# Kernel optimization log

Hardware: AMD Instinct MI355X
Metric: run time of the kernel (lower is better)

The kernel has to match this reference:

```python
import jax, jax.numpy as jnp
import numpy as np

MAX_USERS = 100000
T = 2            # edge_type_count
D = 100          # edge_dim
B = 512
IN_DIM = 200
OUT_DIM = 200
PARTS = [[3, 15], [3, 15, 105, 945]]   # per-schema neighbor partition sizes
RAND_PARTS = [3, 15]
TOTAL_P = sum(PARTS[0]) + sum(PARTS[1])


def _layernorm(x, g, b, eps=1e-6):
    mu = x.mean(axis=-1, keepdims=True)
    var = ((x - mu) ** 2).mean(axis=-1, keepdims=True)
    return (x - mu) / jnp.sqrt(var + eps) * g + b


def _mha(x, Wq, Wk, Wv, Wf, g, b):
    # single-head attention over the second-to-last axis (n_head=1, d_k=d_v=D).
    # NOTE: original only layer-norms q (k, v use the raw input); residual add at end.
    residual = x
    q = _layernorm(x, g, b) @ Wq
    k = x @ Wk
    v = x @ Wv
    attn = jax.nn.softmax(jnp.einsum('...qd,...kd->...qk', q / jnp.sqrt(D), k), axis=-1)
    out = jnp.einsum('...qk,...kd->...qd', attn, v) @ Wf
    return out + residual, attn


def _mean_agg(Ws, Wn, self_x, neigh_x):
    # GraphSAGE-style mean aggregator: relu(concat(self @ Ws, mean(neigh) @ Wn)).
    # neigh_x has shape [N*r, D]; reshape to [N, r, D] and mean over the fanout r.
    n, d = self_x.shape
    neigh_mean = neigh_x.reshape(n, -1, d).mean(axis=1)
    return jax.nn.relu(jnp.concatenate([self_x @ Ws, neigh_mean @ Wn], axis=-1))


def _schema_view(idx, parts, Wself, Wneigh, type_embed, nodeids, neigh_s):
    # neigh_s: [B, T, sum(parts)] node ids for meta-path idx. Returns [B, T, D].
    # Faithful to type_embed[neigh][:, :, :, :, idx, :][:, t, :, t, :] but gathers
    # only the needed (type t, schema idx) slice instead of the huge dense tensor.
    chunks = jnp.split(neigh_s, np.cumsum(parts)[:-1].tolist(), axis=2)
    specs = []
    for t in range(T):
        feats = [type_embed[nodeids, t, idx]]                    # [B, D]
        for c in chunks:
            feats.append(type_embed[c[:, t, :], t, idx].reshape(-1, D))
        for l in range(len(parts)):
            feats = [_mean_agg(Wself[l], Wneigh[l], feats[k], feats[k + 1])
                     for k in range(len(feats) - 1)]
        specs.append(feats[0])
    return jnp.stack(specs, axis=1)


def setup_inputs() -> dict:
    ks = jax.random.split(jax.random.key(0), 32)
    unif = lambda i, s: jax.random.uniform(ks[i], s, dtype=jnp.float32, minval=-1.0, maxval=1.0)
    nrm = lambda i, s, sc=0.1: jax.random.normal(ks[i], s, dtype=jnp.float32) * sc
    inp = {}
    inp['nodeids'] = jax.random.randint(ks[0], (B,), 0, MAX_USERS)
    inp['edgetype'] = jnp.stack([jnp.arange(B), jax.random.randint(ks[1], (B,), 0, T)])
    inp['neighbors'] = jax.random.randint(ks[2], (B, T, TOTAL_P), 0, MAX_USERS)
    inp['random_neighbors'] = jax.random.randint(ks[3], (B, sum(RAND_PARTS)), 0, MAX_USERS)
    inp['base_embed'] = unif(4, (MAX_USERS, IN_DIM))
    inp['type_embed'] = unif(5, (MAX_USERS, T, len(PARTS), D))
    inp['rw_embed'] = unif(6, (MAX_USERS, D))
    inp['reflect'] = nrm(7, (T, D, OUT_DIM), 1.0 / float(np.sqrt(IN_DIM)))
    inp['agg0_self'] = nrm(8, (2, D, D // 2)); inp['agg0_neigh'] = nrm(9, (2, D, D // 2))
    inp['agg1_self'] = nrm(10, (4, D, D // 2)); inp['agg1_neigh'] = nrm(11, (4, D, D // 2))
    inp['rand_self'] = nrm(12, (2, D, D // 2)); inp['rand_neigh'] = nrm(13, (2, D, D // 2))
    inp['vWq'] = nrm(14, (D, D)); inp['vWk'] = nrm(15, (D, D)); inp['vWv'] = nrm(16, (D, D)); inp['vWf'] = nrm(17, (D, D))
    inp['vg'] = jnp.ones((D,), jnp.float32); inp['vb'] = jnp.zeros((D,), jnp.float32)
    inp['mWq'] = nrm(18, (D, D)); inp['mWk'] = nrm(19, (D, D)); inp['mWv'] = nrm(20, (D, D)); inp['mWf'] = nrm(21, (D, D))
    inp['mg'] = jnp.ones((D,), jnp.float32); inp['mb'] = jnp.zeros((D,), jnp.float32)
    return inp


def reference(nodeids, edgetype, neighbors, random_neighbors, base_embed, type_embed,
              rw_embed, reflect, agg0_self, agg0_neigh, agg1_self, agg1_neigh,
              rand_self, rand_neigh, vWq, vWk, vWv, vWf, vg, vb,
              mWq, mWk, mWv, mWf, mg, mb):
    # per-metapath views [B, T, D]
    spec0 = _schema_view(0, PARTS[0], agg0_self, agg0_neigh, type_embed, nodeids,
                         neighbors[:, :, :sum(PARTS[0])])
    spec1 = _schema_view(1, PARTS[1], agg1_self, agg1_neigh, type_embed, nodeids,
                         neighbors[:, :, sum(PARTS[0]):])
    # random-walk view [B, D]
    feats = [rw_embed[nodeids]]
    for c in jnp.split(random_neighbors, np.cumsum(RAND_PARTS)[:-1].tolist(), axis=1):
        feats.append(rw_embed[c].reshape(-1, D))
    for l in range(len(RAND_PARTS)):
        feats = [_mean_agg(rand_self[l], rand_neigh[l], feats[k], feats[k + 1])
                 for k in range(len(feats) - 1)]
    rview = feats[0]
    mv = jnp.stack([spec0, spec1], axis=1)                                   # [B, 2, T, D]
    mv = jnp.concatenate([mv, jnp.broadcast_to(rview[:, None, None, :], (B, 1, T, D))], axis=1)  # [B, 3, T, D]
    mv, _ = _mha(mv, vWq, vWk, vWv, vWf, vg, vb)                             # view attn over type axis T
    mt, _ = _mha(jnp.swapaxes(mv, 1, 2), mWq, mWk, mWv, mWf, mg, mb)         # meta attn over view axis
    pooled = jnp.swapaxes(mt, 1, 2).mean(axis=1)                             # [B, T, D]
    sel = pooled[edgetype[0], edgetype[1]]                                   # [B, D]
    out = jnp.einsum('bd,bdo->bo', sel, reflect[edgetype[1]])                # [B, OUT_DIM]
    res = base_embed[nodeids] + out
    return res / jnp.maximum(jnp.linalg.norm(res, axis=1, keepdims=True), 1e-12)
```

## Files before the change

### kernel.cpp

```cpp
#include <hip/hip_runtime.h>
#include <math.h>


#define NBATCH 512
#define TOTALP 1086
#define RPB 32
#define XSTR 204

struct Seg {
  const float* emb;
  const float* selfp;
  const float* neighp;
  const int*   ids_s;
  const int*   ids_n;
  const float* Ws;
  const float* Wn;
  float*       outp;
  int ss, so;
  int ns, no;
  int estride;
  int ostride;
  int c;
  int r;
  int blk_begin;
};

struct KArgs { Seg seg[14]; int n; };

__global__ __launch_bounds__(256, 5) void agg_kernel(KArgs P) {
  __shared__ float xsh[RPB * XSTR];
  __shared__ int   ids_s_sh[RPB];
  __shared__ int   ids_n_sh[RPB * 9];

  const int blk = blockIdx.x, tid = threadIdx.x;
  int si = 0;
  for (int i = 1; i < P.n; ++i)
    if (blk >= P.seg[i].blk_begin) si = i;
  const Seg sg = P.seg[si];
  const int j0 = (blk - sg.blk_begin) * RPB;
  const int c = sg.c, r = sg.r;

  if (sg.emb) {
    if (tid < RPB) {
      int j = j0 + tid, b = j / c, pos = j - b * c;
      ids_s_sh[tid] = sg.ids_s[(long)b * sg.ss + sg.so + pos];
    }
    for (int u = tid; u < RPB * r; u += 256) {
      int row = u / r, q = u - row * r;
      int j = j0 + row, b = j / c, pos = j - b * c;
      ids_n_sh[u] = sg.ids_n[(long)b * sg.ns + sg.no + pos * r + q];
    }
  }
  __syncthreads();

  const float rinv = 1.f / (float)r;
  for (int u = tid; u < RPB * 25; u += 256) {
    int row = u / 25, q4 = (u - row * 25) * 4;
    float sx, sy, sz, sw, mx = 0.f, my = 0.f, mz = 0.f, mw = 0.f;
    if (sg.emb) {
      const float4 s4 = *(const float4*)(sg.emb + (long)ids_s_sh[row] * sg.estride + q4);
      sx = s4.x; sy = s4.y; sz = s4.z; sw = s4.w;
      for (int rr = 0; rr < r; ++rr) {
        const float4 t = *(const float4*)(sg.emb + (long)ids_n_sh[row * r + rr] * sg.estride + q4);
        mx += t.x; my += t.y; mz += t.z; mw += t.w;
      }
    } else {
      long j = j0 + row;
      const float4 s4 = *(const float4*)(sg.selfp + j * 100 + q4);
      sx = s4.x; sy = s4.y; sz = s4.z; sw = s4.w;
      for (int rr = 0; rr < r; ++rr) {
        const float4 t = *(const float4*)(sg.neighp + (j * r + rr) * 100 + q4);
        mx += t.x; my += t.y; mz += t.z; mw += t.w;
      }
    }
    float4 sv; sv.x = sx; sv.y = sy; sv.z = sz; sv.w = sw;
    float4 mv; mv.x = mx * rinv; mv.y = my * rinv; mv.z = mz * rinv; mv.w = mw * rinv;
    *(float4*)&xsh[row * XSTR + q4]       = sv;
    *(float4*)&xsh[row * XSTR + 100 + q4] = mv;
  }
  __syncthreads();

  if (tid < 224) {
    const int rg = tid / 28, cq = tid - rg * 28;
    const int cl = (cq < 14) ? cq : cq - 14;
    const float* Wg = (cq < 14) ? sg.Ws : sg.Wn;
    const int c0 = (cl < 13) ? 4 * cl : 0;
    const int c1 = (cl < 12) ? c0 + 2 : c0;
    const int xoff = (cq < 14) ? 0 : 100;
    float acc[4][4];
#pragma unroll
    for (int i = 0; i < 4; ++i) { acc[i][0] = acc[i][1] = acc[i][2] = acc[i][3] = 0.f; }
    const float* xb = &xsh[(rg * 4) * XSTR + xoff];
#pragma unroll 4
    for (int e = 0; e < 100; ++e) {
      const float2 w0 = *(const float2*)&Wg[e * 50 + c0];
      const float2 w1 = *(const float2*)&Wg[e * 50 + c1];
#pragma unroll
      for (int i = 0; i < 4; ++i) {
        const float a = xb[i * XSTR + e];
        acc[i][0] = fmaf(a, w0.x, acc[i][0]);
        acc[i][1] = fmaf(a, w0.y, acc[i][1]);
        acc[i][2] = fmaf(a, w1.x, acc[i][2]);
        acc[i][3] = fmaf(a, w1.y, acc[i][3]);
      }
    }
    if (cl < 13) {
      const int cbase = (cq < 14 ? 0 : 50) + 4 * cl;
      for (int i = 0; i < 4; ++i) {
        const long j = j0 + rg * 4 + i;
        float* op = sg.outp + j * (long)sg.ostride + cbase;
        if (cl < 12) {
          float4 o;
          o.x = fmaxf(acc[i][0], 0.f); o.y = fmaxf(acc[i][1], 0.f);
          o.z = fmaxf(acc[i][2], 0.f); o.w = fmaxf(acc[i][3], 0.f);
          *(float4*)op = o;
        } else {
          op[0] = fmaxf(acc[i][0], 0.f);
          op[1] = fmaxf(acc[i][1], 0.f);
        }
      }
    }
  }
}

__device__ __forceinline__ void attn_step(
    float* xs, int base, int rs, int n,
    const float* Wq, const float* Wk, const float* Wv, const float* Wf,
    const float* g, const float* bb,
    float* ln, float* qq, float* kk, float* vv, float* ot,
    float* sc, float* musd, float* wsh, int tid)
{
  if (tid < n) {
    float mu = 0.f;
    for (int d = 0; d < 100; ++d) mu += xs[base + tid * rs + d];
    mu *= 0.01f;
    float var = 0.f;
    for (int d = 0; d < 100; ++d) {
      float t = xs[base + tid * rs + d] - mu; var = fmaf(t, t, var);
    }
    var *= 0.01f;
    musd[tid * 2]     = mu;
    musd[tid * 2 + 1] = rsqrtf(var + 1e-6f);
  }
  __syncthreads();
  for (int o = tid; o < n * 100; o += 128) {
    int i = o / 100, d = o - i * 100;
    ln[o] = (xs[base + i * rs + d] - musd[i * 2]) * musd[i * 2 + 1] * g[d] + bb[d];
  }
  __syncthreads();

  const bool act = tid < n * 25;
  const int  i   = tid / 25;
  const int  d4  = 4 * (tid - i * 25);
  float aq[4] = {0,0,0,0}, ak[4] = {0,0,0,0}, av[4] = {0,0,0,0};
  for (int ch = 0; ch < 2; ++ch) {
    for (int u = tid; u < 1250; u += 128) {
      int el = u / 25, dd = 4 * (u - el * 25);
      *(float4*)&wsh[el * 300 + dd]       = *(const float4*)&Wq[(ch * 50 + el) * 100 + dd];
      *(float4*)&wsh[el * 300 + 100 + dd] = *(const float4*)&Wk[(ch * 50 + el) * 100 + dd];
      *(float4*)&wsh[el * 300 + 200 + dd] = *(const float4*)&Wv[(ch * 50 + el) * 100 + dd];
    }
    __syncthreads();
    if (act) {
      for (int el = 0; el < 50; ++el) {
        const float lnv = ln[i * 100 + ch * 50 + el];
        const float xv  = xs[base + i * rs + ch * 50 + el];
        const float4 wq = *(const float4*)&wsh[el * 300 + d4];
        const float4 wk = *(const float4*)&wsh[el * 300 + 100 + d4];
        const float4 wv = *(const float4*)&wsh[el * 300 + 200 + d4];
        aq[0] = fmaf(lnv, wq.x, aq[0]); aq[1] = fmaf(lnv, wq.y, aq[1]);
        aq[2] = fmaf(lnv, wq.z, aq[2]); aq[3] = fmaf(lnv, wq.w, aq[3]);
        ak[0] = fmaf(xv,  wk.x, ak[0]); ak[1] = fmaf(xv,  wk.y, ak[1]);
        ak[2] = fmaf(xv,  wk.z, ak[2]); ak[3] = fmaf(xv,  wk.w, ak[3]);
        av[0] = fmaf(xv,  wv.x, av[0]); av[1] = fmaf(xv,  wv.y, av[1]);
        av[2] = fmaf(xv,  wv.z, av[2]); av[3] = fmaf(xv,  wv.w, av[3]);
      }
    }
    __syncthreads();
  }
  if (act) {
#pragma unroll
    for (int jj = 0; jj < 4; ++jj) {
      qq[i * 100 + d4 + jj] = aq[jj];
      kk[i * 100 + d4 + jj] = ak[jj];
      vv[i * 100 + d4 + jj] = av[jj];
    }
  }
  __syncthreads();

  if (tid < n * n) {
    int qi = tid / n, u = tid - qi * n;
    float s = 0.f;
    for (int d = 0; d < 100; ++d) s = fmaf(qq[qi * 100 + d], kk[u * 100 + d], s);
    sc[tid] = s * 0.1f;
  }
  __syncthreads();
  if (tid < n) {
    float mx = sc[tid * n];
    for (int u = 1; u < n; ++u) mx = fmaxf(mx, sc[tid * n + u]);
    float sm = 0.f;
    for (int u = 0; u < n; ++u) {
      float e = expf(sc[tid * n + u] - mx); sc[tid * n + u] = e; sm += e;
    }
    float inv = 1.f / sm;
    for (int u = 0; u < n; ++u) sc[tid * n + u] *= inv;
  }
  __syncthreads();
  for (int o = tid; o < n * 100; o += 128) {
    int ii = o / 100, d = o - ii * 100;
    float a = 0.f;
    for (int u = 0; u < n; ++u) a = fmaf(sc[ii * n + u], vv[u * 100 + d], a);
    ot[o] = a;
  }
  __syncthreads();

  float af[4] = {0,0,0,0};
  for (int ch = 0; ch < 2; ++ch) {
    for (int u = tid; u < 1250; u += 128) {
      int el = u / 25, dd = 4 * (u - el * 25);
      *(float4*)&wsh[el * 100 + dd] = *(const float4*)&Wf[(ch * 50 + el) * 100 + dd];
    }
    __syncthreads();
    if (act) {
      for (int el = 0; el < 50; ++el) {
        const float ov = ot[i * 100 + ch * 50 + el];
        const float4 wf = *(const float4*)&wsh[el * 100 + d4];
        af[0] = fmaf(ov, wf.x, af[0]); af[1] = fmaf(ov, wf.y, af[1]);
        af[2] = fmaf(ov, wf.z, af[2]); af[3] = fmaf(ov, wf.w, af[3]);
      }
    }
    __syncthreads();
  }
  if (act) {
#pragma unroll
    for (int jj = 0; jj < 4; ++jj)
      xs[base + i * rs + d4 + jj] += af[jj];
  }
  __syncthreads();
}

__global__ __launch_bounds__(128) void attn_final_kernel(
    const float* __restrict__ spec, const float* __restrict__ rview,
    const int* __restrict__ nodeids, const int* __restrict__ edgetype,
    const float* __restrict__ base_embed, const float* __restrict__ reflect,
    const float* vWq, const float* vWk, const float* vWv, const float* vWf,
    const float* vg, const float* vb,
    const float* mWq, const float* mWk, const float* mWv, const float* mWf,
    const float* mg, const float* mb,
    float* __restrict__ out)
{
  __shared__ float xs[600], ln[300], qq[300], kk[300], vv[300], ot[300];
  __shared__ float sc[9], musd[6], r200[200], pooled[200], nrmv[1];
  __shared__ float wsh[15000];
  const int b = blockIdx.x, tid = threadIdx.x;

  for (int o = tid; o < 600; o += 128) {
    int v = o / 200, rem = o - v * 200;
    xs[o] = (v < 2) ? spec[(long)b * 400 + o] : rview[(long)b * 100 + (rem % 100)];
  }
  __syncthreads();

  for (int v = 0; v < 3; ++v)
    attn_step(xs, v * 200, 100, 2, vWq, vWk, vWv, vWf, vg, vb,
              ln, qq, kk, vv, ot, sc, musd, wsh, tid);
  for (int t = 0; t < 2; ++t)
    attn_step(xs, t * 100, 200, 3, mWq, mWk, mWv, mWf, mg, mb,
              ln, qq, kk, vv, ot, sc, musd, wsh, tid);

  for (int o = tid; o < 200; o += 128)
    pooled[o] = (xs[o] + xs[200 + o] + xs[400 + o]) * (1.f / 3.f);
  __syncthreads();

  const int  et  = edgetype[NBATCH + b];
  const long nid = nodeids[b];

  float ar[4] = {0,0,0,0};
  if (tid < 50) {
    const float4 be = *(const float4*)&base_embed[nid * 200 + 4 * tid];
    ar[0] = be.x; ar[1] = be.y; ar[2] = be.z; ar[3] = be.w;
  }
  for (int ch = 0; ch < 2; ++ch) {
    for (int u = tid; u < 2500; u += 128) {
      int dl = u / 50, oo = 4 * (u - dl * 50);
      *(float4*)&wsh[dl * 200 + oo] =
          *(const float4*)&reflect[((long)et * 100 + ch * 50 + dl) * 200 + oo];
    }
    __syncthreads();
    if (tid < 50) {
      for (int dl = 0; dl < 50; ++dl) {
        const float pv = pooled[et * 100 + ch * 50 + dl];
        const float4 rv = *(const float4*)&wsh[dl * 200 + 4 * tid];
        ar[0] = fmaf(pv, rv.x, ar[0]); ar[1] = fmaf(pv, rv.y, ar[1]);
        ar[2] = fmaf(pv, rv.z, ar[2]); ar[3] = fmaf(pv, rv.w, ar[3]);
      }
    }
    __syncthreads();
  }
  if (tid < 50) {
    r200[4 * tid]     = ar[0]; r200[4 * tid + 1] = ar[1];
    r200[4 * tid + 2] = ar[2]; r200[4 * tid + 3] = ar[3];
  }
  __syncthreads();
  if (tid == 0) {
    float ss = 0.f;
    for (int o = 0; o < 200; ++o) ss = fmaf(r200[o], r200[o], ss);
    nrmv[0] = 1.f / fmaxf(sqrtf(ss), 1e-12f);
  }
  __syncthreads();
  for (int o = tid; o < 200; o += 128)
    out[(long)b * 200 + o] = r200[o] * nrmv[0];
}

extern "C" void kernel_launch(void* const* d_in, const int* in_sizes, int n_in,
                              void* d_out, int out_size, void* d_ws, size_t ws_size,
                              hipStream_t stream) {
  (void)in_sizes; (void)n_in; (void)out_size; (void)ws_size;
  const int*   nodeids          = (const int*)d_in[0];
  const int*   edgetype         = (const int*)d_in[1];
  const int*   neighbors        = (const int*)d_in[2];
  const int*   random_neighbors = (const int*)d_in[3];
  const float* base_embed       = (const float*)d_in[4];
  const float* type_embed       = (const float*)d_in[5];
  const float* rw_embed         = (const float*)d_in[6];
  const float* reflect          = (const float*)d_in[7];
  const float* agg0_self        = (const float*)d_in[8];
  const float* agg0_neigh       = (const float*)d_in[9];
  const float* agg1_self        = (const float*)d_in[10];
  const float* agg1_neigh       = (const float*)d_in[11];
  const float* rand_self        = (const float*)d_in[12];
  const float* rand_neigh       = (const float*)d_in[13];
  const float* vWq = (const float*)d_in[14];
  const float* vWk = (const float*)d_in[15];
  const float* vWv = (const float*)d_in[16];
  const float* vWf = (const float*)d_in[17];
  const float* vg  = (const float*)d_in[18];
  const float* vb  = (const float*)d_in[19];
  const float* mWq = (const float*)d_in[20];
  const float* mWk = (const float*)d_in[21];
  const float* mWv = (const float*)d_in[22];
  const float* mWf = (const float*)d_in[23];
  const float* mg  = (const float*)d_in[24];
  const float* mb  = (const float*)d_in[25];

  float* ws = (float*)d_ws;
  const long S1r = 147L * NBATCH;
  auto rp = [&](long rows) { return ws + rows * 100; };
  float* spec_f  = ws + 306L * NBATCH * 100;
  float* rview_f = spec_f + (long)NBATCH * 400;

  const int  OFF1[4] = {18, 21, 36, 141};
  const int  FAN1[4] = {3, 5, 7, 9};
  const int  C1[4]   = {1, 3, 15, 105};
  const long CUM1[4]  = {0, 1, 4, 19};
  const long CUM1b[3] = {0, 1, 4};

  KArgs A; long acc = 0;
  auto addg = [&](const float* emb, int estride,
                  const int* isrc, int ss, int so, int c,
                  const int* insrc, int nstr, int no, int r,
                  const float* Ws, const float* Wn, float* outp, int ostride) {
    Seg& s = A.seg[A.n++];
    s.emb = emb; s.selfp = nullptr; s.neighp = nullptr;
    s.ids_s = isrc; s.ids_n = insrc;
    s.Ws = Ws; s.Wn = Wn; s.outp = outp;
    s.ss = ss; s.so = so; s.ns = nstr; s.no = no;
    s.estride = estride; s.ostride = ostride;
    s.c = c; s.r = r; s.blk_begin = (int)acc;
    acc += (long)c * NBATCH / RPB;
  };
  auto addd = [&](const float* selfp, const float* neighp, int c, int r,
                  const float* Ws, const float* Wn, float* outp, int ostride) {
    Seg& s = A.seg[A.n++];
    s.emb = nullptr; s.selfp = selfp; s.neighp = neighp;
    s.ids_s = nullptr; s.ids_n = nullptr;
    s.Ws = Ws; s.Wn = Wn; s.outp = outp;
    s.ss = 0; s.so = 0; s.ns = 0; s.no = 0; s.estride = 0; s.ostride = ostride;
    s.c = c; s.r = r; s.blk_begin = (int)acc;
    acc += (long)c * NBATCH / RPB;
  };

  A.n = 0; acc = 0;
  for (int t = 0; t < 2; ++t)
    for (int k = 0; k < 4; ++k) {
      const float* emb = type_embed + (t * 2 + 1) * 100;
      if (k == 0)
        addg(emb, 400, nodeids, 1, 0, 1,
             neighbors, 2 * TOTALP, t * TOTALP + OFF1[k], FAN1[k],
             agg1_self, agg1_neigh, rp(t * S1r + CUM1[k] * NBATCH), 100);
      else
        addg(emb, 400, neighbors, 2 * TOTALP, t * TOTALP + OFF1[k - 1], C1[k],
             neighbors, 2 * TOTALP, t * TOTALP + OFF1[k], FAN1[k],
             agg1_self, agg1_neigh, rp(t * S1r + CUM1[k] * NBATCH), 100);
    }
  for (int t = 0; t < 2; ++t)
    for (int k = 0; k < 2; ++k) {
      const float* emb = type_embed + (t * 2 + 0) * 100;
      long obase = 294L * NBATCH + (long)t * 4 * NBATCH + (k == 0 ? 0 : 1) * NBATCH;
      if (k == 0)
        addg(emb, 400, nodeids, 1, 0, 1,
             neighbors, 2 * TOTALP, t * TOTALP + 0, 3,
             agg0_self, agg0_neigh, rp(obase), 100);
      else
        addg(emb, 400, neighbors, 2 * TOTALP, t * TOTALP + 0, 3,
             neighbors, 2 * TOTALP, t * TOTALP + 3, 5,
             agg0_self, agg0_neigh, rp(obase), 100);
    }
  for (int k = 0; k < 2; ++k) {
    long obase = 302L * NBATCH + (k == 0 ? 0 : 1) * NBATCH;
    if (k == 0)
      addg(rw_embed, 100, nodeids, 1, 0, 1,
           random_neighbors, 18, 0, 3, rand_self, rand_neigh, rp(obase), 100);
    else
      addg(rw_embed, 100, random_neighbors, 18, 0, 3,
           random_neighbors, 18, 3, 5, rand_self, rand_neigh, rp(obase), 100);
  }
  agg_kernel<<<dim3((unsigned)acc), dim3(256), 0, stream>>>(A);

  A.n = 0; acc = 0;
  for (int t = 0; t < 2; ++t)
    for (int k = 0; k < 3; ++k)
      addd(rp(t * S1r + CUM1[k] * NBATCH), rp(t * S1r + CUM1[k + 1] * NBATCH),
           C1[k], FAN1[k], agg1_self + 5000, agg1_neigh + 5000,
           rp(t * S1r + 124L * NBATCH + CUM1b[k] * NBATCH), 100);
  for (int t = 0; t < 2; ++t)
    addd(rp(294L * NBATCH + (long)t * 4 * NBATCH),
         rp(294L * NBATCH + (long)t * 4 * NBATCH + NBATCH),
         1, 3, agg0_self + 5000, agg0_neigh + 5000, spec_f + t * 100, 400);
  addd(rp(302L * NBATCH), rp(303L * NBATCH), 1, 3,
       rand_self + 5000, rand_neigh + 5000, rview_f, 100);
  agg_kernel<<<dim3((unsigned)acc), dim3(256), 0, stream>>>(A);

  A.n = 0; acc = 0;
  for (int t = 0; t < 2; ++t)
    for (int k = 0; k < 2; ++k)
      addd(rp(t * S1r + 124L * NBATCH + CUM1b[k] * NBATCH),
           rp(t * S1r + 124L * NBATCH + CUM1b[k + 1] * NBATCH),
           C1[k], FAN1[k], agg1_self + 10000, agg1_neigh + 10000,
           rp(t * S1r + 143L * NBATCH + (k == 0 ? 0 : 1) * NBATCH), 100);
  agg_kernel<<<dim3((unsigned)acc), dim3(256), 0, stream>>>(A);

  A.n = 0; acc = 0;
  for (int t = 0; t < 2; ++t)
    addd(rp(t * S1r + 143L * NBATCH), rp(t * S1r + 144L * NBATCH),
         1, 3, agg1_self + 15000, agg1_neigh + 15000,
         spec_f + 200 + t * 100, 400);
  agg_kernel<<<dim3((unsigned)acc), dim3(256), 0, stream>>>(A);

  attn_final_kernel<<<dim3(NBATCH), dim3(128), 0, stream>>>(
      spec_f, rview_f, nodeids, edgetype, base_embed, reflect,
      vWq, vWk, vWv, vWf, vg, vb, mWq, mWk, mWv, mWf, mg, mb,
      (float*)d_out);
}
```

Measured before the change: 639.8 us.

## Split aggregation kernel into gather/dense variants with templated fanout; drop attention weight staging

The single aggregation kernel is split into a gather variant (embedding lookups by id) and a dense variant (reading prior-layer outputs). The fanout loop is templated on R so it can be fully unrolled, and launch bounds change from 5 to 4 blocks per SM. The attention/final kernel no longer stages weight matrices in a 60KB shared buffer and instead reads weights directly from global memory via restrict pointers. This removes many block-wide barriers and raises occupancy, at the cost of relying on cache for repeated weight reads.

```diff
diff --git a/kernel.cpp b/kernel.cpp
--- a/kernel.cpp
+++ b/kernel.cpp
@@ -27,59 +27,8 @@
 
 struct KArgs { Seg seg[14]; int n; };
 
-__global__ __launch_bounds__(256, 5) void agg_kernel(KArgs P) {
-  __shared__ float xsh[RPB * XSTR];
-  __shared__ int   ids_s_sh[RPB];
-  __shared__ int   ids_n_sh[RPB * 9];
-
-  const int blk = blockIdx.x, tid = threadIdx.x;
-  int si = 0;
-  for (int i = 1; i < P.n; ++i)
-    if (blk >= P.seg[i].blk_begin) si = i;
-  const Seg sg = P.seg[si];
-  const int j0 = (blk - sg.blk_begin) * RPB;
-  const int c = sg.c, r = sg.r;
-
-  if (sg.emb) {
-    if (tid < RPB) {
-      int j = j0 + tid, b = j / c, pos = j - b * c;
-      ids_s_sh[tid] = sg.ids_s[(long)b * sg.ss + sg.so + pos];
-    }
-    for (int u = tid; u < RPB * r; u += 256) {
-      int row = u / r, q = u - row * r;
-      int j = j0 + row, b = j / c, pos = j - b * c;
-      ids_n_sh[u] = sg.ids_n[(long)b * sg.ns + sg.no + pos * r + q];
-    }
-  }
-  __syncthreads();
-
-  const float rinv = 1.f / (float)r;
-  for (int u = tid; u < RPB * 25; u += 256) {
-    int row = u / 25, q4 = (u - row * 25) * 4;
-    float sx, sy, sz, sw, mx = 0.f, my = 0.f, mz = 0.f, mw = 0.f;
-    if (sg.emb) {
-      const float4 s4 = *(const float4*)(sg.emb + (long)ids_s_sh[row] * sg.estride + q4);
-      sx = s4.x; sy = s4.y; sz = s4.z; sw = s4.w;
-      for (int rr = 0; rr < r; ++rr) {
-        const float4 t = *(const float4*)(sg.emb + (long)ids_n_sh[row * r + rr] * sg.estride + q4);
-        mx += t.x; my += t.y; mz += t.z; mw += t.w;
-      }
-    } else {
-      long j = j0 + row;
-      const float4 s4 = *(const float4*)(sg.selfp + j * 100 + q4);
-      sx = s4.x; sy = s4.y; sz = s4.z; sw = s4.w;
-      for (int rr = 0; rr < r; ++rr) {
-        const float4 t = *(const float4*)(sg.neighp + (j * r + rr) * 100 + q4);
-        mx += t.x; my += t.y; mz += t.z; mw += t.w;
-      }
-    }
-    float4 sv; sv.x = sx; sv.y = sy; sv.z = sz; sv.w = sw;
-    float4 mv; mv.x = mx * rinv; mv.y = my * rinv; mv.z = mz * rinv; mv.w = mw * rinv;
-    *(float4*)&xsh[row * XSTR + q4]       = sv;
-    *(float4*)&xsh[row * XSTR + 100 + q4] = mv;
-  }
-  __syncthreads();
-
+__device__ __forceinline__ void phaseC(const Seg& sg, int j0, int tid,
+                                       const float* xsh) {
   if (tid < 224) {
     const int rg = tid / 28, cq = tid - rg * 28;
     const int cl = (cq < 14) ? cq : cq - 14;
@@ -123,12 +72,106 @@
   }
 }
 
+template <int R>
+__device__ __forceinline__ void phaseB_g(const Seg& sg, int tid, float* xsh,
+                                         const int* ids_s_sh, const int* ids_n_sh) {
+  const float rinv = 1.f / (float)R;
+  for (int u = tid; u < RPB * 25; u += 256) {
+    const int row = u / 25, q4 = (u - row * 25) * 4;
+    float4 s4 = *(const float4*)(sg.emb + (long)ids_s_sh[row] * sg.estride + q4);
+    float mx = 0.f, my = 0.f, mz = 0.f, mw = 0.f;
+#pragma unroll
+    for (int rr = 0; rr < R; ++rr) {
+      const float4 t = *(const float4*)(sg.emb + (long)ids_n_sh[row * R + rr] * sg.estride + q4);
+      mx += t.x; my += t.y; mz += t.z; mw += t.w;
+    }
+    *(float4*)&xsh[row * XSTR + q4] = s4;
+    float4 mv; mv.x = mx * rinv; mv.y = my * rinv; mv.z = mz * rinv; mv.w = mw * rinv;
+    *(float4*)&xsh[row * XSTR + 100 + q4] = mv;
+  }
+}
+
+template <int R>
+__device__ __forceinline__ void phaseB_d(const Seg& sg, int j0, int tid, float* xsh) {
+  const float rinv = 1.f / (float)R;
+  for (int u = tid; u < RPB * 25; u += 256) {
+    const int row = u / 25, q4 = (u - row * 25) * 4;
+    const long j = j0 + row;
+    float4 s4 = *(const float4*)(sg.selfp + j * 100 + q4);
+    float mx = 0.f, my = 0.f, mz = 0.f, mw = 0.f;
+#pragma unroll
+    for (int rr = 0; rr < R; ++rr) {
+      const float4 t = *(const float4*)(sg.neighp + (j * R + rr) * 100 + q4);
+      mx += t.x; my += t.y; mz += t.z; mw += t.w;
+    }
+    *(float4*)&xsh[row * XSTR + q4] = s4;
+    float4 mv; mv.x = mx * rinv; mv.y = my * rinv; mv.z = mz * rinv; mv.w = mw * rinv;
+    *(float4*)&xsh[row * XSTR + 100 + q4] = mv;
+  }
+}
+
+__global__ __launch_bounds__(256, 4) void agg_gather(KArgs P) {
+  __shared__ float xsh[RPB * XSTR];
+  __shared__ int   ids_s_sh[RPB];
+  __shared__ int   ids_n_sh[RPB * 9];
+
+  const int blk = blockIdx.x, tid = threadIdx.x;
+  int si = 0;
+  for (int i = 1; i < P.n; ++i)
+    if (blk >= P.seg[i].blk_begin) si = i;
+  const Seg sg = P.seg[si];
+  const int j0 = (blk - sg.blk_begin) * RPB;
+  const int c = sg.c, r = sg.r;
+
+  if (tid < RPB) {
+    int j = j0 + tid, b = j / c, pos = j - b * c;
+    ids_s_sh[tid] = sg.ids_s[(long)b * sg.ss + sg.so + pos];
+  }
+  for (int u = tid; u < RPB * r; u += 256) {
+    int row = u / r, q = u - row * r;
+    int j = j0 + row, b = j / c, pos = j - b * c;
+    ids_n_sh[u] = sg.ids_n[(long)b * sg.ns + sg.no + pos * r + q];
+  }
+  __syncthreads();
+
+  switch (r) {
+    case 3: phaseB_g<3>(sg, tid, xsh, ids_s_sh, ids_n_sh); break;
+    case 5: phaseB_g<5>(sg, tid, xsh, ids_s_sh, ids_n_sh); break;
+    case 7: phaseB_g<7>(sg, tid, xsh, ids_s_sh, ids_n_sh); break;
+    default: phaseB_g<9>(sg, tid, xsh, ids_s_sh, ids_n_sh); break;
+  }
+  __syncthreads();
+
+  phaseC(sg, j0, tid, xsh);
+}
+
+__global__ __launch_bounds__(256, 4) void agg_dense(KArgs P) {
+  __shared__ float xsh[RPB * XSTR];
+
+  const int blk = blockIdx.x, tid = threadIdx.x;
+  int si = 0;
+  for (int i = 1; i < P.n; ++i)
+    if (blk >= P.seg[i].blk_begin) si = i;
+  const Seg sg = P.seg[si];
+  const int j0 = (blk - sg.blk_begin) * RPB;
+
+  switch (sg.r) {
+    case 3: phaseB_d<3>(sg, j0, tid, xsh); break;
+    case 5: phaseB_d<5>(sg, j0, tid, xsh); break;
+    default: phaseB_d<7>(sg, j0, tid, xsh); break;
+  }
+  __syncthreads();
+
+  phaseC(sg, j0, tid, xsh);
+}
+
 __device__ __forceinline__ void attn_step(
     float* xs, int base, int rs, int n,
-    const float* Wq, const float* Wk, const float* Wv, const float* Wf,
-    const float* g, const float* bb,
+    const float* __restrict__ Wq, const float* __restrict__ Wk,
+    const float* __restrict__ Wv, const float* __restrict__ Wf,
+    const float* __restrict__ g, const float* __restrict__ bb,
     float* ln, float* qq, float* kk, float* vv, float* ot,
-    float* sc, float* musd, float* wsh, int tid)
+    float* sc, float* musd, int tid)
 {
   if (tid < n) {
     float mu = 0.f;
@@ -152,33 +195,22 @@
   const bool act = tid < n * 25;
   const int  i   = tid / 25;
   const int  d4  = 4 * (tid - i * 25);
-  float aq[4] = {0,0,0,0}, ak[4] = {0,0,0,0}, av[4] = {0,0,0,0};
-  for (int ch = 0; ch < 2; ++ch) {
-    for (int u = tid; u < 1250; u += 128) {
-      int el = u / 25, dd = 4 * (u - el * 25);
-      *(float4*)&wsh[el * 300 + dd]       = *(const float4*)&Wq[(ch * 50 + el) * 100 + dd];
-      *(float4*)&wsh[el * 300 + 100 + dd] = *(const float4*)&Wk[(ch * 50 + el) * 100 + dd];
-      *(float4*)&wsh[el * 300 + 200 + dd] = *(const float4*)&Wv[(ch * 50 + el) * 100 + dd];
-    }
-    __syncthreads();
-    if (act) {
-      for (int el = 0; el < 50; ++el) {
-        const float lnv = ln[i * 100 + ch * 50 + el];
-        const float xv  = xs[base + i * rs + ch * 50 + el];
-        const float4 wq = *(const float4*)&wsh[el * 300 + d4];
-        const float4 wk = *(const float4*)&wsh[el * 300 + 100 + d4];
-        const float4 wv = *(const float4*)&wsh[el * 300 + 200 + d4];
-        aq[0] = fmaf(lnv, wq.x, aq[0]); aq[1] = fmaf(lnv, wq.y, aq[1]);
-        aq[2] = fmaf(lnv, wq.z, aq[2]); aq[3] = fmaf(lnv, wq.w, aq[3]);
-        ak[0] = fmaf(xv,  wk.x, ak[0]); ak[1] = fmaf(xv,  wk.y, ak[1]);
-        ak[2] = fmaf(xv,  wk.z, ak[2]); ak[3] = fmaf(xv,  wk.w, ak[3]);
-        av[0] = fmaf(xv,  wv.x, av[0]); av[1] = fmaf(xv,  wv.y, av[1]);
-        av[2] = fmaf(xv,  wv.z, av[2]); av[3] = fmaf(xv,  wv.w, av[3]);
-      }
-    }
-    __syncthreads();
-  }
   if (act) {
+    float aq[4] = {0,0,0,0}, ak[4] = {0,0,0,0}, av[4] = {0,0,0,0};
+#pragma unroll 4
+    for (int el = 0; el < 100; ++el) {
+      const float lnv = ln[i * 100 + el];
+      const float xv  = xs[base + i * rs + el];
+      const float4 wq = *(const float4*)&Wq[el * 100 + d4];
+      const float4 wk = *(const float4*)&Wk[el * 100 + d4];
+      const float4 wv = *(const float4*)&Wv[el * 100 + d4];
+      aq[0] = fmaf(lnv, wq.x, aq[0]); aq[1] = fmaf(lnv, wq.y, aq[1]);
+      aq[2] = fmaf(lnv, wq.z, aq[2]); aq[3] = fmaf(lnv, wq.w, aq[3]);
+      ak[0] = fmaf(xv,  wk.x, ak[0]); ak[1] = fmaf(xv,  wk.y, ak[1]);
+      ak[2] = fmaf(xv,  wk.z, ak[2]); ak[3] = fmaf(xv,  wk.w, ak[3]);
+      av[0] = fmaf(xv,  wv.x, av[0]); av[1] = fmaf(xv,  wv.y, av[1]);
+      av[2] = fmaf(xv,  wv.z, av[2]); av[3] = fmaf(xv,  wv.w, av[3]);
+    }
 #pragma unroll
     for (int jj = 0; jj < 4; ++jj) {
       qq[i * 100 + d4 + jj] = aq[jj];
@@ -214,24 +246,15 @@
   }
   __syncthreads();
 
-  float af[4] = {0,0,0,0};
-  for (int ch = 0; ch < 2; ++ch) {
-    for (int u = tid; u < 1250; u += 128) {
-      int el = u / 25, dd = 4 * (u - el * 25);
-      *(float4*)&wsh[el * 100 + dd] = *(const float4*)&Wf[(ch * 50 + el) * 100 + dd];
-    }
-    __syncthreads();
-    if (act) {
-      for (int el = 0; el < 50; ++el) {
-        const float ov = ot[i * 100 + ch * 50 + el];
-        const float4 wf = *(const float4*)&wsh[el * 100 + d4];
-        af[0] = fmaf(ov, wf.x, af[0]); af[1] = fmaf(ov, wf.y, af[1]);
-        af[2] = fmaf(ov, wf.z, af[2]); af[3] = fmaf(ov, wf.w, af[3]);
-      }
-    }
-    __syncthreads();
-  }
   if (act) {
+    float af[4] = {0,0,0,0};
+#pragma unroll 4
+    for (int el = 0; el < 100; ++el) {
+      const float ov = ot[i * 100 + el];
+      const float4 wf = *(const float4*)&Wf[el * 100 + d4];
+      af[0] = fmaf(ov, wf.x, af[0]); af[1] = fmaf(ov, wf.y, af[1]);
+      af[2] = fmaf(ov, wf.z, af[2]); af[3] = fmaf(ov, wf.w, af[3]);
+    }
 #pragma unroll
     for (int jj = 0; jj < 4; ++jj)
       xs[base + i * rs + d4 + jj] += af[jj];
@@ -243,15 +266,16 @@
     const float* __restrict__ spec, const float* __restrict__ rview,
     const int* __restrict__ nodeids, const int* __restrict__ edgetype,
     const float* __restrict__ base_embed, const float* __restrict__ reflect,
-    const float* vWq, const float* vWk, const float* vWv, const float* vWf,
-    const float* vg, const float* vb,
-    const float* mWq, const float* mWk, const float* mWv, const float* mWf,
-    const float* mg, const float* mb,
+    const float* __restrict__ vWq, const float* __restrict__ vWk,
+    const float* __restrict__ vWv, const float* __restrict__ vWf,
+    const float* __restrict__ vg, const float* __restrict__ vb,
+    const float* __restrict__ mWq, const float* __restrict__ mWk,
+    const float* __restrict__ mWv, const float* __restrict__ mWf,
+    const float* __restrict__ mg, const float* __restrict__ mb,
     float* __restrict__ out)
 {
   __shared__ float xs[600], ln[300], qq[300], kk[300], vv[300], ot[300];
   __shared__ float sc[9], musd[6], r200[200], pooled[200], nrmv[1];
-  __shared__ float wsh[15000];
   const int b = blockIdx.x, tid = threadIdx.x;
 
   for (int o = tid; o < 600; o += 128) {
@@ -262,10 +286,10 @@
 
   for (int v = 0; v < 3; ++v)
     attn_step(xs, v * 200, 100, 2, vWq, vWk, vWv, vWf, vg, vb,
-              ln, qq, kk, vv, ot, sc, musd, wsh, tid);
+              ln, qq, kk, vv, ot, sc, musd, tid);
   for (int t = 0; t < 2; ++t)
     attn_step(xs, t * 100, 200, 3, mWq, mWk, mWv, mWf, mg, mb,
-              ln, qq, kk, vv, ot, sc, musd, wsh, tid);
+              ln, qq, kk, vv, ot, sc, musd, tid);
 
   for (int o = tid; o < 200; o += 128)
     pooled[o] = (xs[o] + xs[200 + o] + xs[400 + o]) * (1.f / 3.f);
@@ -278,25 +302,13 @@
   if (tid < 50) {
     const float4 be = *(const float4*)&base_embed[nid * 200 + 4 * tid];
     ar[0] = be.x; ar[1] = be.y; ar[2] = be.z; ar[3] = be.w;
-  }
-  for (int ch = 0; ch < 2; ++ch) {
-    for (int u = tid; u < 2500; u += 128) {
-      int dl = u / 50, oo = 4 * (u - dl * 50);
-      *(float4*)&wsh[dl * 200 + oo] =
-          *(const float4*)&reflect[((long)et * 100 + ch * 50 + dl) * 200 + oo];
-    }
-    __syncthreads();
-    if (tid < 50) {
-      for (int dl = 0; dl < 50; ++dl) {
-        const float pv = pooled[et * 100 + ch * 50 + dl];
-        const float4 rv = *(const float4*)&wsh[dl * 200 + 4 * tid];
-        ar[0] = fmaf(pv, rv.x, ar[0]); ar[1] = fmaf(pv, rv.y, ar[1]);
-        ar[2] = fmaf(pv, rv.z, ar[2]); ar[3] = fmaf(pv, rv.w, ar[3]);
-      }
-    }
-    __syncthreads();
-  }
-  if (tid < 50) {
+#pragma unroll 4
+    for (int dl = 0; dl < 100; ++dl) {
+      const float pv = pooled[et * 100 + dl];
+      const float4 rv = *(const float4*)&reflect[((long)et * 100 + dl) * 200 + 4 * tid];
+      ar[0] = fmaf(pv, rv.x, ar[0]); ar[1] = fmaf(pv, rv.y, ar[1]);
+      ar[2] = fmaf(pv, rv.z, ar[2]); ar[3] = fmaf(pv, rv.w, ar[3]);
+    }
     r200[4 * tid]     = ar[0]; r200[4 * tid + 1] = ar[1];
     r200[4 * tid + 2] = ar[2]; r200[4 * tid + 3] = ar[3];
   }
@@ -414,7 +426,7 @@
       addg(rw_embed, 100, random_neighbors, 18, 0, 3,
            random_neighbors, 18, 3, 5, rand_self, rand_neigh, rp(obase), 100);
   }
-  agg_kernel<<<dim3((unsigned)acc), dim3(256), 0, stream>>>(A);
+  agg_gather<<<dim3((unsigned)acc), dim3(256), 0, stream>>>(A);
 
   A.n = 0; acc = 0;
   for (int t = 0; t < 2; ++t)
@@ -428,7 +440,7 @@
          1, 3, agg0_self + 5000, agg0_neigh + 5000, spec_f + t * 100, 400);
   addd(rp(302L * NBATCH), rp(303L * NBATCH), 1, 3,
        rand_self + 5000, rand_neigh + 5000, rview_f, 100);
-  agg_kernel<<<dim3((unsigned)acc), dim3(256), 0, stream>>>(A);
+  agg_dense<<<dim3((unsigned)acc), dim3(256), 0, stream>>>(A);
 
   A.n = 0; acc = 0;
   for (int t = 0; t < 2; ++t)
@@ -437,14 +449,14 @@
            rp(t * S1r + 124L * NBATCH + CUM1b[k + 1] * NBATCH),
            C1[k], FAN1[k], agg1_self + 10000, agg1_neigh + 10000,
            rp(t * S1r + 143L * NBATCH + (k == 0 ? 0 : 1) * NBATCH), 100);
-  agg_kernel<<<dim3((unsigned)acc), dim3(256), 0, stream>>>(A);
+  agg_dense<<<dim3((unsigned)acc), dim3(256), 0, stream>>>(A);
 
   A.n = 0; acc = 0;
   for (int t = 0; t < 2; ++t)
     addd(rp(t * S1r + 143L * NBATCH), rp(t * S1r + 144L * NBATCH),
          1, 3, agg1_self + 15000, agg1_neigh + 15000,
          spec_f + 200 + t * 100, 400);
-  agg_kernel<<<dim3((unsigned)acc), dim3(256), 0, stream>>>(A);
+  agg_dense<<<dim3((unsigned)acc), dim3(256), 0, stream>>>(A);
 
   attn_final_kernel<<<dim3(NBATCH), dim3(128), 0, stream>>>(
       spec_f, rview_f, nodeids, edgetype, base_embed, reflect,
```

Measured after the change: 617.8 us. 3.4% less time.
